# Performance work log

Hardware: AMD Instinct MI355X
Metric: run time of the kernel (lower is better)

Reference implementation:

```python
import jax, jax.numpy as jnp
import numpy as np

VOCAB, HIDDEN, BATCH, T = 32000, 256, 16, 256


def setup_inputs() -> dict:
    key = jax.random.key(0)
    ks = jax.random.split(key, 8)
    s_in = 1.0 / np.sqrt(HIDDEN)  # torch nn.RNN init scale (1/sqrt(hidden))
    inputs = jax.random.randint(ks[0], (BATCH, T), 0, VOCAB)
    targets = jax.random.randint(ks[1], (BATCH, T), 0, VOCAB)
    # RNN params: torch stores W_ih as (hidden, vocab); we keep the transpose
    # (vocab, hidden) so one_hot(x) @ W_ih.T == Wih[x] (an exact gather).
    Wih = jax.random.uniform(ks[2], (VOCAB, HIDDEN), minval=-s_in, maxval=s_in)
    bih = jax.random.uniform(ks[3], (HIDDEN,), minval=-s_in, maxval=s_in)
    Whh = jax.random.uniform(ks[4], (HIDDEN, HIDDEN), minval=-s_in, maxval=s_in)
    bhh = jax.random.uniform(ks[5], (HIDDEN,), minval=-s_in, maxval=s_in)
    Wfc = jax.random.uniform(ks[6], (VOCAB, HIDDEN), minval=-s_in, maxval=s_in)
    bfc = jax.random.uniform(ks[7], (VOCAB,), minval=-s_in, maxval=s_in)
    return {"inputs": inputs, "targets": targets, "Wih": Wih, "bih": bih,
            "Whh": Whh, "bhh": bhh, "Wfc": Wfc, "bfc": bfc}


def reference(inputs, targets, Wih, bih, Whh, bhh, Wfc, bfc):
    # one_hot(inputs) @ W_ih.T + b_ih  ==  Wih[inputs] + bih (exact same math)
    xproj = Wih[inputs] + bih                      # (B, T, H)
    B = inputs.shape[0]
    h0 = jnp.zeros((B, HIDDEN), dtype=Wih.dtype)

    def step(h, xt):
        h = jnp.tanh(xt + h @ Whh.T + bhh)
        return h, h

    _, hs = jax.lax.scan(step, h0, jnp.swapaxes(xproj, 0, 1))  # (T, B, H)
    hs = jnp.swapaxes(hs, 0, 1)                    # (B, T, H)
    logits = hs @ Wfc.T + bfc                      # (B, T, V)
    logp = jax.nn.log_softmax(logits, axis=-1)
    nll = -jnp.take_along_axis(logp, targets[..., None], axis=-1)
    return jnp.mean(nll)                           # scalar cross-entropy loss
```

## Files before the change

### kernel.cpp

```cpp
#include <hip/hip_runtime.h>
#include <hip/hip_bf16.h>
#include <stdint.h>

#define VOCAB 32000
#define HID   256
#define BATCH 16
#define SEQT  256
#define ROWS  (BATCH*SEQT)

typedef __attribute__((ext_vector_type(8))) short bf16x8_t;
typedef __attribute__((ext_vector_type(4))) float f32x4_t;

__device__ __forceinline__ short f2bs(float x) {
    __hip_bfloat16 h = __float2bfloat16(x);
    return *reinterpret_cast<short*>(&h);
}
__device__ __forceinline__ bf16x8_t cvt8(float4 a, float4 b) {
    union { short s[8]; bf16x8_t v; } u;
    u.s[0] = f2bs(a.x); u.s[1] = f2bs(a.y); u.s[2] = f2bs(a.z); u.s[3] = f2bs(a.w);
    u.s[4] = f2bs(b.x); u.s[5] = f2bs(b.y); u.s[6] = f2bs(b.z); u.s[7] = f2bs(b.w);
    return u.v;
}
__device__ __forceinline__ void barrier_lds() {
    asm volatile("s_waitcnt lgkmcnt(0)\n\ts_barrier" ::: "memory");
}
__device__ __forceinline__ float tanh_exp(float x) {
    float e = __builtin_amdgcn_exp2f(x * 2.885390081777927f);
    return fmaf(-2.f, __builtin_amdgcn_rcpf(e + 1.f), 1.f);
}
__device__ __forceinline__ uint32_t pk_bf16(float lo, float hi) {
    uint32_t r;
    asm("v_cvt_pk_bf16_f32 %0, %1, %2" : "=v"(r) : "v"(lo), "v"(hi));
    return r;
}
__device__ __forceinline__ void gload_lds16(const short* g, short* lds_base) {
    __builtin_amdgcn_global_load_lds(
        (const __attribute__((address_space(1))) void*)g,
        (__attribute__((address_space(3))) void*)lds_base, 16, 0, 0);
}


__global__ __launch_bounds__(256) void xproj_kernel(
    const int* __restrict__ inputs,
    const float* __restrict__ Wih,
    const float* __restrict__ bih,
    const float* __restrict__ bhh,
    float* __restrict__ xp,
    float* __restrict__ S)
{
    int idx = blockIdx.x * 256 + threadIdx.x;
    int h  = idx & 255;
    int tb = idx >> 8;
    int b  = tb & 15;
    int t  = tb >> 4;
    int id = inputs[b * SEQT + t];
    xp[idx] = Wih[(size_t)id * HID + h] + bih[h] + bhh[h];
    if (idx < ROWS) S[idx] = 0.0f;
}

__device__ void rnn_core(const float* __restrict__ xp,
                         const float* __restrict__ Whh,
                         __hip_bfloat16* __restrict__ hs)
{
    __shared__ __align__(8) short hbuf[2][16][264];
    const int tid = threadIdx.x;
    const int l = tid & 63, w = tid >> 6;
    const int lr = l & 15, lh = l >> 4;
    const int n0 = w * 32 + lr * 2;
    short* hsg = (short*)hs + (n0 >> 5) * 512 + (((n0 >> 3) & 3) * 128) + (n0 & 7);

    bf16x8_t bfrag[2][8];
#pragma unroll
    for (int nt = 0; nt < 2; nt++)
#pragma unroll
        for (int ki = 0; ki < 8; ki++) {
            const float4* p = (const float4*)(Whh + (size_t)(n0 + nt) * HID + ki * 32 + lh * 8);
            bfrag[nt][ki] = cvt8(p[0], p[1]);
        }
    for (int i = tid; i < 16 * 264; i += 512) ((short*)hbuf[0])[i] = 0;
    __syncthreads();

    float2 xva[4], xvb[4];
#pragma unroll
    for (int r = 0; r < 4; r++)
        xva[r] = *(const float2*)(xp + (lh * 4 + r) * HID + n0);

    auto step = [&](int SRC, int DST, float2* xc, float2* xn, int t) {
        bf16x8_t afr[8];
#pragma unroll
        for (int ki = 0; ki < 8; ki++)
            afr[ki] = *(const bf16x8_t*)(&hbuf[SRC][lr][ki * 32 + lh * 8]);

        f32x4_t a0a = {xc[0].x, xc[1].x, xc[2].x, xc[3].x};
        f32x4_t a1a = {xc[0].y, xc[1].y, xc[2].y, xc[3].y};
        f32x4_t a0b = {0.f, 0.f, 0.f, 0.f};
        f32x4_t a1b = {0.f, 0.f, 0.f, 0.f};
#pragma unroll
        for (int ki = 0; ki < 4; ki++) {
            a0a = __builtin_amdgcn_mfma_f32_16x16x32_bf16(afr[ki],     bfrag[0][ki],     a0a, 0, 0, 0);
            a0b = __builtin_amdgcn_mfma_f32_16x16x32_bf16(afr[ki + 4], bfrag[0][ki + 4], a0b, 0, 0, 0);
            a1a = __builtin_amdgcn_mfma_f32_16x16x32_bf16(afr[ki],     bfrag[1][ki],     a1a, 0, 0, 0);
            a1b = __builtin_amdgcn_mfma_f32_16x16x32_bf16(afr[ki + 4], bfrag[1][ki + 4], a1b, 0, 0, 0);
        }

        if (t + 1 < SEQT) {
            const float* xb = xp + (size_t)(t + 1) * (BATCH * HID);
#pragma unroll
            for (int r = 0; r < 4; r++)
                xn[r] = *(const float2*)(xb + (lh * 4 + r) * HID + n0);
        }

#pragma unroll
        for (int r = 0; r < 4; r++) {
            float v0 = a0a[r] + a0b[r];
            float v1 = a1a[r] + a1b[r];
            uint32_t pk = pk_bf16(tanh_exp(v0), tanh_exp(v1));
            *(uint32_t*)(&hbuf[DST][lh * 4 + r][n0]) = pk;
            *(uint32_t*)(hsg + (size_t)t * 4096 + (lh * 4 + r) * 8) = pk;
        }
        barrier_lds();
    };

    for (int t = 0; t < SEQT; t += 2) {
        step(0, 1, xva, xvb, t);
        step(1, 0, xvb, xva, t + 1);
    }
}

__global__ __launch_bounds__(512, 1) void rnncvt_kernel(
    const float* __restrict__ xp,
    const float* __restrict__ Whh,
    __hip_bfloat16* __restrict__ hs,
    const float* __restrict__ Wfc,
    __hip_bfloat16* __restrict__ Wfcb,
    int do_cvt)
{
    if (blockIdx.x == 0) { rnn_core(xp, Whh, hs); return; }
    if (!do_cvt) return;
    for (int idx = (int)(blockIdx.x - 1) * 512 + threadIdx.x;
         idx < (VOCAB * HID / 8); idx += 256 * 512) {
        int e   = idx * 8;
        int m   = (e >> 3) & 15;
        int lhh = (e >> 7) & 3;
        int ki  = (e >> 9) & 7;
        int tile = e >> 12;
        const float4* p = (const float4*)(Wfc + (size_t)(tile * 16 + m) * HID
                                          + ki * 32 + lhh * 8);
        *(bf16x8_t*)((short*)Wfcb + (size_t)e) = cvt8(p[0], p[1]);
    }
}

template <bool BF16B>
__global__ __launch_bounds__(256) void fc_kernel(
    const __hip_bfloat16* __restrict__ hsz,
    const void* __restrict__ WfcP,
    const float* __restrict__ bfc,
    const int* __restrict__ targets,
    float* __restrict__ S,
    float* __restrict__ TL)
{
    __shared__ __align__(16) short As[2][8 * 512];
    __shared__ __align__(16) short Bs[2][8 * 512];
    __shared__ int tgt[128];

    const int bid = blockIdx.x;
    const int xcd = bid & 7;
    const int j   = bid >> 3;
    const int m_id = j & 31;
    const int n_id = (j >> 5) * 8 + xcd;
    if (n_id >= VOCAB / 128) return;
    const int m0 = m_id * 128, n0 = n_id * 128;

    const int tid = threadIdx.x;
    const int l = tid & 63, w = tid >> 6;
    const int lr = l & 15, lh = l >> 4;
    const int wm = (w >> 1) * 64, wn = (w & 1) * 64;

    if (tid < 128) {
        int r = m0 + tid;
        tgt[tid] = targets[((r & 15) << 8) | (r >> 4)];
    }
    __builtin_amdgcn_sched_barrier(0);

    const short* Ag = (const short*)hsz + (size_t)m_id * 32768 + (size_t)(w * 2) * 4096 + l * 8;
    const short* Bg = (const short*)WfcP + (size_t)n_id * 32768 + (size_t)(w * 2) * 4096 + l * 8;
    const float* Bf = (const float*)WfcP;

    f32x4_t acc[4][4];
    const f32x4_t z = {0.f, 0.f, 0.f, 0.f};
#pragma unroll
    for (int i = 0; i < 4; i++)
#pragma unroll
        for (int jj = 0; jj < 4; jj++) acc[i][jj] = z;

    if (BF16B) {
        auto stage = [&](int buf, int s) {
            gload_lds16(Ag + s * 512,        &As[buf][(w * 2) * 512]);
            gload_lds16(Ag + 4096 + s * 512, &As[buf][(w * 2 + 1) * 512]);
            gload_lds16(Bg + s * 512,        &Bs[buf][(w * 2) * 512]);
            gload_lds16(Bg + 4096 + s * 512, &Bs[buf][(w * 2 + 1) * 512]);
        };
        stage(0, 0);
        stage(1, 1);
        __builtin_amdgcn_sched_barrier(0);

#pragma unroll
        for (int s = 0; s < 8; s++) {
            const int buf = s & 1;
            if (s < 7) asm volatile("s_waitcnt vmcnt(4)\n\ts_barrier" ::: "memory");
            else       asm volatile("s_waitcnt vmcnt(0)\n\ts_barrier" ::: "memory");

            bf16x8_t a[4], b[4];
#pragma unroll
            for (int mt = 0; mt < 4; mt++)
                a[mt] = *(const bf16x8_t*)&As[buf][(((w >> 1) * 4 + mt) * 512) + l * 8];
#pragma unroll
            for (int nt = 0; nt < 4; nt++)
                b[nt] = *(const bf16x8_t*)&Bs[buf][(((w & 1) * 4 + nt) * 512) + l * 8];

            if (s < 6) {
                barrier_lds();
                stage(buf, s + 2);
                __builtin_amdgcn_sched_barrier(0);
            }
#pragma unroll
            for (int mt = 0; mt < 4; mt++)
#pragma unroll
                for (int nt = 0; nt < 4; nt++)
                    acc[mt][nt] = __builtin_amdgcn_mfma_f32_16x16x32_bf16(
                        a[mt], b[nt], acc[mt][nt], 0, 0, 0);
        }
    } else {
        for (int s = 0; s < 8; s++) {
            __syncthreads();
#pragma unroll
            for (int i = 0; i < 2; i++) {
                int tt = w * 2 + i;
                bf16x8_t va = *(const bf16x8_t*)(Ag + i * 4096 + s * 512);
                *(bf16x8_t*)&As[0][tt * 512 + l * 8] = va;
                int n = n0 + tt * 16 + lr;
                const float4* p = (const float4*)(Bf + (size_t)n * HID + s * 32 + lh * 8);
                *(bf16x8_t*)&Bs[0][tt * 512 + l * 8] = cvt8(p[0], p[1]);
            }
            __syncthreads();
            bf16x8_t a[4], b[4];
#pragma unroll
            for (int mt = 0; mt < 4; mt++)
                a[mt] = *(const bf16x8_t*)&As[0][(((w >> 1) * 4 + mt) * 512) + l * 8];
#pragma unroll
            for (int nt = 0; nt < 4; nt++)
                b[nt] = *(const bf16x8_t*)&Bs[0][(((w & 1) * 4 + nt) * 512) + l * 8];
#pragma unroll
            for (int mt = 0; mt < 4; mt++)
#pragma unroll
                for (int nt = 0; nt < 4; nt++)
                    acc[mt][nt] = __builtin_amdgcn_mfma_f32_16x16x32_bf16(
                        a[mt], b[nt], acc[mt][nt], 0, 0, 0);
        }
    }

    int tg[16];
#pragma unroll
    for (int i = 0; i < 16; i++)
        tg[i] = tgt[wm + (i >> 2) * 16 + lh * 4 + (i & 3)];

    float rsum[16];
#pragma unroll
    for (int i = 0; i < 16; i++) rsum[i] = 0.f;
#pragma unroll
    for (int nt = 0; nt < 4; nt++) {
        int n = n0 + wn + nt * 16 + lr;
        float bias = bfc[n];
#pragma unroll
        for (int mt = 0; mt < 4; mt++)
#pragma unroll
            for (int r = 0; r < 4; r++) {
                float v = acc[mt][nt][r] + bias;
                rsum[mt * 4 + r] += __expf(v);
                if (tg[mt * 4 + r] == n)
                    TL[m0 + wm + mt * 16 + lh * 4 + r] = v;
            }
    }
#pragma unroll
    for (int m = 1; m < 16; m <<= 1)
#pragma unroll
        for (int i = 0; i < 16; i++) rsum[i] += __shfl_xor(rsum[i], m, 64);
    if (lr == 0) {
#pragma unroll
        for (int i = 0; i < 16; i++) {
            int r = m0 + wm + (i >> 2) * 16 + lh * 4 + (i & 3);
            atomicAdd(&S[r], rsum[i]);
        }
    }
}

__global__ __launch_bounds__(256) void loss_kernel(
    const float* __restrict__ S,
    const float* __restrict__ TL,
    float* __restrict__ out)
{
    int tid = threadIdx.x;
    float p = 0.f;
    for (int i = tid; i < ROWS; i += 256) p += __logf(S[i]) - TL[i];
#pragma unroll
    for (int m = 1; m < 64; m <<= 1) p += __shfl_xor(p, m, 64);
    __shared__ float red[4];
    if ((tid & 63) == 0) red[tid >> 6] = p;
    __syncthreads();
    if (tid == 0)
        out[0] = (red[0] + red[1] + red[2] + red[3]) / (float)ROWS;
}

extern "C" void kernel_launch(void* const* d_in, const int* in_sizes, int n_in,
                              void* d_out, int out_size, void* d_ws, size_t ws_size,
                              hipStream_t stream)
{
    (void)in_sizes; (void)n_in; (void)out_size;
    const int*   inputs  = (const int*)d_in[0];
    const int*   targets = (const int*)d_in[1];
    const float* Wih = (const float*)d_in[2];
    const float* bih = (const float*)d_in[3];
    const float* Whh = (const float*)d_in[4];
    const float* bhh = (const float*)d_in[5];
    const float* Wfc = (const float*)d_in[6];
    const float* bfc = (const float*)d_in[7];

    float* S  = (float*)d_ws;
    float* TL = S + ROWS;
    float* xp = TL + ROWS;
    __hip_bfloat16* hs = (__hip_bfloat16*)(xp + (size_t)SEQT * BATCH * HID);
    __hip_bfloat16* Wfcb = hs + (size_t)ROWS * HID;

    const size_t need = (size_t)(2 * ROWS) * 4 + (size_t)ROWS * HID * 4
                      + (size_t)ROWS * HID * 2 + (size_t)VOCAB * HID * 2;
    const int use_bf16b = (ws_size >= need) ? 1 : 0;

    xproj_kernel<<<(SEQT * BATCH * HID) / 256, 256, 0, stream>>>(
        inputs, Wih, bih, bhh, xp, S);
    rnncvt_kernel<<<257, 512, 0, stream>>>(xp, Whh, hs, Wfc, Wfcb, use_bf16b);
    if (use_bf16b)
        fc_kernel<true><<<8192, 256, 0, stream>>>(hs, (const void*)Wfcb, bfc, targets, S, TL);
    else
        fc_kernel<false><<<8192, 256, 0, stream>>>(hs, (const void*)Wfc, bfc, targets, S, TL);
    loss_kernel<<<1, 256, 0, stream>>>(S, TL, (float*)d_out);
}
```

Measured before the change: 442.1 us.

## Use weight-stationary FC kernel with per-block partial sums and two-stage loss reduction

Replaces the 8192-block tiled FC GEMM with a 250-block kernel. Each block keeps its 128-column slice of the bf16 Wfc in registers and streams all hidden-state rows through double-buffered LDS. Softmax denominators are accumulated per block in LDS, written as per-block partials into the reused xp buffer, and reduced by two new loss kernels, which removes the global atomics and the repeated B-tile reloads. The RNN also now writes hs to global with coalesced 16-byte stores one step late, read back from LDS, instead of scattered 4-byte stores. The trade-offs are only 250 blocks of parallelism, high register pressure, and an extra launch.

```diff
diff --git a/kernel.cpp b/kernel.cpp
--- a/kernel.cpp
+++ b/kernel.cpp
@@ -62,12 +62,14 @@
                          const float* __restrict__ Whh,
                          __hip_bfloat16* __restrict__ hs)
 {
-    __shared__ __align__(8) short hbuf[2][16][264];
+    __shared__ short hbuf[2][16][264];
     const int tid = threadIdx.x;
     const int l = tid & 63, w = tid >> 6;
     const int lr = l & 15, lh = l >> 4;
+    const int cm = tid >> 5;
+    const int cc = (tid & 31) * 8;
     const int n0 = w * 32 + lr * 2;
-    short* hsg = (short*)hs + (n0 >> 5) * 512 + (((n0 >> 3) & 3) * 128) + (n0 & 7);
+    const int cpoff = ((cc >> 5) * 512) + (((cc >> 3) & 3) * 128) + cm * 8;
 
     bf16x8_t bfrag[2][8];
 #pragma unroll
@@ -86,6 +88,10 @@
         xva[r] = *(const float2*)(xp + (lh * 4 + r) * HID + n0);
 
     auto step = [&](int SRC, int DST, float2* xc, float2* xn, int t) {
+        if (t > 0) {
+            bf16x8_t hv = *(const bf16x8_t*)(&hbuf[SRC][cm][cc]);
+            *(bf16x8_t*)((short*)hs + (size_t)(t - 1) * 4096 + cpoff) = hv;
+        }
         bf16x8_t afr[8];
 #pragma unroll
         for (int ki = 0; ki < 8; ki++)
@@ -116,7 +122,6 @@
             float v1 = a1a[r] + a1b[r];
             uint32_t pk = pk_bf16(tanh_exp(v0), tanh_exp(v1));
             *(uint32_t*)(&hbuf[DST][lh * 4 + r][n0]) = pk;
-            *(uint32_t*)(hsg + (size_t)t * 4096 + (lh * 4 + r) * 8) = pk;
         }
         barrier_lds();
     };
@@ -125,6 +130,8 @@
         step(0, 1, xva, xvb, t);
         step(1, 0, xvb, xva, t + 1);
     }
+    bf16x8_t hv = *(const bf16x8_t*)(&hbuf[0][cm][cc]);
+    *(bf16x8_t*)((short*)hs + (size_t)(SEQT - 1) * 4096 + cpoff) = hv;
 }
 
 __global__ __launch_bounds__(512, 1) void rnncvt_kernel(
@@ -150,17 +157,164 @@
     }
 }
 
-template <bool BF16B>
-__global__ __launch_bounds__(256) void fc_kernel(
+__global__ __launch_bounds__(512, 1) void fc_sb_kernel(
     const __hip_bfloat16* __restrict__ hsz,
-    const void* __restrict__ WfcP,
+    const __hip_bfloat16* __restrict__ Wfcb,
+    const float* __restrict__ bfc,
+    const int* __restrict__ targets,
+    float* __restrict__ Sp,
+    float* __restrict__ TL)
+{
+    __shared__ __align__(16) short As[2 * 4 * 8 * 512];
+    __shared__ float rsum[ROWS];
+    __shared__ int tgtb[2][64];
+
+    const int j = blockIdx.x;
+    const int tid = threadIdx.x;
+    const int l = tid & 63, w = tid >> 6;
+    const int lr = l & 15, lh = l >> 4;
+    const int wr = w >> 1;
+    const int wc = w & 1;
+
+    bf16x8_t Br0[8], Br1[8], Br2[8], Br3[8];
+    {
+        const short* BW = (const short*)Wfcb + (size_t)(j * 8 + wc * 4) * 4096 + l * 8;
+#pragma unroll
+        for (int ki = 0; ki < 8; ki++) {
+            Br0[ki] = *(const bf16x8_t*)(BW + 0 * 4096 + ki * 512);
+            Br1[ki] = *(const bf16x8_t*)(BW + 1 * 4096 + ki * 512);
+            Br2[ki] = *(const bf16x8_t*)(BW + 2 * 4096 + ki * 512);
+            Br3[ki] = *(const bf16x8_t*)(BW + 3 * 4096 + ki * 512);
+        }
+    }
+    const int colbase = j * 128 + wc * 64 + lr;
+    const float bias0 = bfc[colbase];
+    const float bias1 = bfc[colbase + 16];
+    const float bias2 = bfc[colbase + 32];
+    const float bias3 = bfc[colbase + 48];
+
+    for (int i = tid; i < ROWS; i += 512) rsum[i] = 0.f;
+
+    const short* AG = (const short*)hsz;
+    auto stageA = [&](int buf, int m) {
+        const short* src = AG + ((size_t)(m * 4 + wr) * 8 + wc * 4) * 512 + l * 8;
+        short* dst = As + ((buf * 4 + wr) * 8 + wc * 4) * 512;
+#pragma unroll
+        for (int q = 0; q < 4; q++)
+            gload_lds16(src + q * 512, dst + q * 512);
+    };
+
+    stageA(0, 0);
+    if (tid < 64) tgtb[0][tid] = targets[((tid & 15) << 8) | (tid >> 4)];
+    __syncthreads();
+
+    for (int m = 0; m < 64; m++) {
+        const int buf = m & 1;
+        int tnext = 0;
+        if (m < 63) {
+            stageA(buf ^ 1, m + 1);
+            if (tid < 64) {
+                int row = (m + 1) * 64 + tid;
+                tnext = targets[((row & 15) << 8) | (row >> 4)];
+            }
+        }
+
+        f32x4_t acc0 = {0,0,0,0}, acc1 = {0,0,0,0}, acc2 = {0,0,0,0}, acc3 = {0,0,0,0};
+        const short* Ab = As + ((buf * 4 + wr) * 8) * 512 + l * 8;
+#pragma unroll
+        for (int ki = 0; ki < 8; ki++) {
+            bf16x8_t a = *(const bf16x8_t*)(Ab + ki * 512);
+            acc0 = __builtin_amdgcn_mfma_f32_16x16x32_bf16(a, Br0[ki], acc0, 0, 0, 0);
+            acc1 = __builtin_amdgcn_mfma_f32_16x16x32_bf16(a, Br1[ki], acc1, 0, 0, 0);
+            acc2 = __builtin_amdgcn_mfma_f32_16x16x32_bf16(a, Br2[ki], acc2, 0, 0, 0);
+            acc3 = __builtin_amdgcn_mfma_f32_16x16x32_bf16(a, Br3[ki], acc3, 0, 0, 0);
+        }
+
+        const int rowbase = m * 64 + wr * 16 + lh * 4;
+        int4 tg = *(const int4*)&tgtb[buf][wr * 16 + lh * 4];
+        float rs0 = 0.f, rs1 = 0.f, rs2 = 0.f, rs3 = 0.f;
+
+#define FC_EPI(ACC, BIAS, OFF) {                                         \
+        int col = colbase + OFF;                                         \
+        float v0 = ACC[0] + BIAS, v1 = ACC[1] + BIAS;                    \
+        float v2 = ACC[2] + BIAS, v3 = ACC[3] + BIAS;                    \
+        rs0 += __expf(v0); rs1 += __expf(v1);                            \
+        rs2 += __expf(v2); rs3 += __expf(v3);                            \
+        if (tg.x == col) TL[rowbase + 0] = v0;                           \
+        if (tg.y == col) TL[rowbase + 1] = v1;                           \
+        if (tg.z == col) TL[rowbase + 2] = v2;                           \
+        if (tg.w == col) TL[rowbase + 3] = v3; }
+
+        FC_EPI(acc0, bias0, 0)
+        FC_EPI(acc1, bias1, 16)
+        FC_EPI(acc2, bias2, 32)
+        FC_EPI(acc3, bias3, 48)
+#undef FC_EPI
+
+#pragma unroll
+        for (int d = 1; d < 16; d <<= 1) {
+            rs0 += __shfl_xor(rs0, d, 64);
+            rs1 += __shfl_xor(rs1, d, 64);
+            rs2 += __shfl_xor(rs2, d, 64);
+            rs3 += __shfl_xor(rs3, d, 64);
+        }
+        if (lr == 0) {
+            atomicAdd(&rsum[rowbase + 0], rs0);
+            atomicAdd(&rsum[rowbase + 1], rs1);
+            atomicAdd(&rsum[rowbase + 2], rs2);
+            atomicAdd(&rsum[rowbase + 3], rs3);
+        }
+
+        if (m < 63) {
+            if (tid < 64) tgtb[buf ^ 1][tid] = tnext;
+            __syncthreads();
+        }
+    }
+    __syncthreads();
+    float* SpRow = Sp + (size_t)j * ROWS;
+    *(float4*)(SpRow + tid * 8)     = *(const float4*)(rsum + tid * 8);
+    *(float4*)(SpRow + tid * 8 + 4) = *(const float4*)(rsum + tid * 8 + 4);
+}
+
+__global__ __launch_bounds__(256) void loss1_kernel(
+    const float* __restrict__ Sp,
+    const float* __restrict__ TL,
+    float* __restrict__ part)
+{
+    const int tid = threadIdx.x;
+    const int r = blockIdx.x * 256 + tid;
+    float tot = 0.f;
+#pragma unroll 5
+    for (int jj = 0; jj < 250; jj++) tot += Sp[(size_t)jj * ROWS + r];
+    float val = __logf(tot) - TL[r];
+#pragma unroll
+    for (int d = 1; d < 64; d <<= 1) val += __shfl_xor(val, d, 64);
+    __shared__ float red[4];
+    if ((tid & 63) == 0) red[tid >> 6] = val;
+    __syncthreads();
+    if (tid == 0)
+        part[blockIdx.x] = red[0] + red[1] + red[2] + red[3];
+}
+__global__ __launch_bounds__(64) void loss2_kernel(
+    const float* __restrict__ part, float* __restrict__ out)
+{
+    int tid = threadIdx.x;
+    float p = (tid < 16) ? part[tid] : 0.f;
+#pragma unroll
+    for (int d = 1; d < 64; d <<= 1) p += __shfl_xor(p, d, 64);
+    if (tid == 0) out[0] = p / (float)ROWS;
+}
+
+__global__ __launch_bounds__(256) void fc_fb_kernel(
+    const __hip_bfloat16* __restrict__ hsz,
+    const float* __restrict__ Bf,
     const float* __restrict__ bfc,
     const int* __restrict__ targets,
     float* __restrict__ S,
     float* __restrict__ TL)
 {
-    __shared__ __align__(16) short As[2][8 * 512];
-    __shared__ __align__(16) short Bs[2][8 * 512];
+    __shared__ __align__(16) short As[8 * 512];
+    __shared__ __align__(16) short Bs[8 * 512];
     __shared__ int tgt[128];
 
     const int bid = blockIdx.x;
@@ -180,11 +334,7 @@
         int r = m0 + tid;
         tgt[tid] = targets[((r & 15) << 8) | (r >> 4)];
     }
-    __builtin_amdgcn_sched_barrier(0);
-
     const short* Ag = (const short*)hsz + (size_t)m_id * 32768 + (size_t)(w * 2) * 4096 + l * 8;
-    const short* Bg = (const short*)WfcP + (size_t)n_id * 32768 + (size_t)(w * 2) * 4096 + l * 8;
-    const float* Bf = (const float*)WfcP;
 
     f32x4_t acc[4][4];
     const f32x4_t z = {0.f, 0.f, 0.f, 0.f};
@@ -193,77 +343,37 @@
 #pragma unroll
         for (int jj = 0; jj < 4; jj++) acc[i][jj] = z;
 
-    if (BF16B) {
-        auto stage = [&](int buf, int s) {
-            gload_lds16(Ag + s * 512,        &As[buf][(w * 2) * 512]);
-            gload_lds16(Ag + 4096 + s * 512, &As[buf][(w * 2 + 1) * 512]);
-            gload_lds16(Bg + s * 512,        &Bs[buf][(w * 2) * 512]);
-            gload_lds16(Bg + 4096 + s * 512, &Bs[buf][(w * 2 + 1) * 512]);
-        };
-        stage(0, 0);
-        stage(1, 1);
-        __builtin_amdgcn_sched_barrier(0);
-
-#pragma unroll
-        for (int s = 0; s < 8; s++) {
-            const int buf = s & 1;
-            if (s < 7) asm volatile("s_waitcnt vmcnt(4)\n\ts_barrier" ::: "memory");
-            else       asm volatile("s_waitcnt vmcnt(0)\n\ts_barrier" ::: "memory");
-
-            bf16x8_t a[4], b[4];
-#pragma unroll
-            for (int mt = 0; mt < 4; mt++)
-                a[mt] = *(const bf16x8_t*)&As[buf][(((w >> 1) * 4 + mt) * 512) + l * 8];
+    for (int s = 0; s < 8; s++) {
+        __syncthreads();
+#pragma unroll
+        for (int i = 0; i < 2; i++) {
+            int tt = w * 2 + i;
+            bf16x8_t va = *(const bf16x8_t*)(Ag + i * 4096 + s * 512);
+            *(bf16x8_t*)&As[tt * 512 + l * 8] = va;
+            int n = n0 + tt * 16 + lr;
+            const float4* p = (const float4*)(Bf + (size_t)n * HID + s * 32 + lh * 8);
+            *(bf16x8_t*)&Bs[tt * 512 + l * 8] = cvt8(p[0], p[1]);
+        }
+        __syncthreads();
+        bf16x8_t a[4], b[4];
+#pragma unroll
+        for (int mt = 0; mt < 4; mt++)
+            a[mt] = *(const bf16x8_t*)&As[(((w >> 1) * 4 + mt) * 512) + l * 8];
+#pragma unroll
+        for (int nt = 0; nt < 4; nt++)
+            b[nt] = *(const bf16x8_t*)&Bs[(((w & 1) * 4 + nt) * 512) + l * 8];
+#pragma unroll
+        for (int mt = 0; mt < 4; mt++)
 #pragma unroll
             for (int nt = 0; nt < 4; nt++)
-                b[nt] = *(const bf16x8_t*)&Bs[buf][(((w & 1) * 4 + nt) * 512) + l * 8];
-
-            if (s < 6) {
-                barrier_lds();
-                stage(buf, s + 2);
-                __builtin_amdgcn_sched_barrier(0);
-            }
-#pragma unroll
-            for (int mt = 0; mt < 4; mt++)
-#pragma unroll
-                for (int nt = 0; nt < 4; nt++)
-                    acc[mt][nt] = __builtin_amdgcn_mfma_f32_16x16x32_bf16(
-                        a[mt], b[nt], acc[mt][nt], 0, 0, 0);
-        }
-    } else {
-        for (int s = 0; s < 8; s++) {
-            __syncthreads();
-#pragma unroll
-            for (int i = 0; i < 2; i++) {
-                int tt = w * 2 + i;
-                bf16x8_t va = *(const bf16x8_t*)(Ag + i * 4096 + s * 512);
-                *(bf16x8_t*)&As[0][tt * 512 + l * 8] = va;
-                int n = n0 + tt * 16 + lr;
-                const float4* p = (const float4*)(Bf + (size_t)n * HID + s * 32 + lh * 8);
-                *(bf16x8_t*)&Bs[0][tt * 512 + l * 8] = cvt8(p[0], p[1]);
-            }
-            __syncthreads();
-            bf16x8_t a[4], b[4];
-#pragma unroll
-            for (int mt = 0; mt < 4; mt++)
-                a[mt] = *(const bf16x8_t*)&As[0][(((w >> 1) * 4 + mt) * 512) + l * 8];
-#pragma unroll
-            for (int nt = 0; nt < 4; nt++)
-                b[nt] = *(const bf16x8_t*)&Bs[0][(((w & 1) * 4 + nt) * 512) + l * 8];
-#pragma unroll
-            for (int mt = 0; mt < 4; mt++)
-#pragma unroll
-                for (int nt = 0; nt < 4; nt++)
-                    acc[mt][nt] = __builtin_amdgcn_mfma_f32_16x16x32_bf16(
-                        a[mt], b[nt], acc[mt][nt], 0, 0, 0);
-        }
+                acc[mt][nt] = __builtin_amdgcn_mfma_f32_16x16x32_bf16(
+                    a[mt], b[nt], acc[mt][nt], 0, 0, 0);
     }
 
     int tg[16];
 #pragma unroll
     for (int i = 0; i < 16; i++)
         tg[i] = tgt[wm + (i >> 2) * 16 + lh * 4 + (i & 3)];
-
     float rsum[16];
 #pragma unroll
     for (int i = 0; i < 16; i++) rsum[i] = 0.f;
@@ -328,6 +438,7 @@
     float* S  = (float*)d_ws;
     float* TL = S + ROWS;
     float* xp = TL + ROWS;
+    float* Sp = xp;
     __hip_bfloat16* hs = (__hip_bfloat16*)(xp + (size_t)SEQT * BATCH * HID);
     __hip_bfloat16* Wfcb = hs + (size_t)ROWS * HID;
 
@@ -338,9 +449,12 @@
     xproj_kernel<<<(SEQT * BATCH * HID) / 256, 256, 0, stream>>>(
         inputs, Wih, bih, bhh, xp, S);
     rnncvt_kernel<<<257, 512, 0, stream>>>(xp, Whh, hs, Wfc, Wfcb, use_bf16b);
-    if (use_bf16b)
-        fc_kernel<true><<<8192, 256, 0, stream>>>(hs, (const void*)Wfcb, bfc, targets, S, TL);
-    else
-        fc_kernel<false><<<8192, 256, 0, stream>>>(hs, (const void*)Wfc, bfc, targets, S, TL);
-    loss_kernel<<<1, 256, 0, stream>>>(S, TL, (float*)d_out);
-}
+    if (use_bf16b) {
+        fc_sb_kernel<<<250, 512, 0, stream>>>(hs, Wfcb, bfc, targets, Sp, TL);
+        loss1_kernel<<<16, 256, 0, stream>>>(Sp, TL, S);
+        loss2_kernel<<<1, 64, 0, stream>>>(S, (float*)d_out);
+    } else {
+        fc_fb_kernel<<<8192, 256, 0, stream>>>(hs, Wfc, bfc, targets, S, TL);
+        loss_kernel<<<1, 256, 0, stream>>>(S, TL, (float*)d_out);
+    }
+}
```

After: 440.4 us. Within noise of the previous version (-0.4%).

## Pipeline RNN time chunks with FC tiles across fused kernel launches

Applied to the files above, without the earlier changes.

Splits the sequential RNN into four 64-step chunks, each run by block 0 of a fused launch while the other blocks compute FC/log-softmax tiles for the previous chunk's hidden states. The FC tile grows to 128x256 with 512 threads, and hidden-state stores now go through LDS as coalesced 16-byte writes instead of scattered 4-byte writes. The goal is to hide the FC GEMM behind the latency-bound recurrence, at the cost of extra launches and reloading Whh for every chunk.

```diff
diff --git a/kernel.cpp b/kernel.cpp
--- a/kernel.cpp
+++ b/kernel.cpp
@@ -39,6 +39,10 @@
         (__attribute__((address_space(3))) void*)lds_base, 16, 0, 0);
 }
 
+
+struct RnnS { short hbuf[2][16][264]; };
+struct FcS  { short As[2][8][512]; short Bs[2][16][512]; int tgt[128]; };
+union  SMem { RnnS r; FcS f; };
 
 __global__ __launch_bounds__(256) void xproj_kernel(
     const int* __restrict__ inputs,
@@ -58,16 +62,19 @@
     if (idx < ROWS) S[idx] = 0.0f;
 }
 
-__device__ void rnn_core(const float* __restrict__ xp,
-                         const float* __restrict__ Whh,
-                         __hip_bfloat16* __restrict__ hs)
-{
-    __shared__ __align__(8) short hbuf[2][16][264];
+__device__ void rnn_chunk(const float* __restrict__ xp,
+                          const float* __restrict__ Whh,
+                          __hip_bfloat16* __restrict__ hs,
+                          int t0, int t1, RnnS& rs)
+{
+    auto& hbuf = rs.hbuf;
     const int tid = threadIdx.x;
     const int l = tid & 63, w = tid >> 6;
     const int lr = l & 15, lh = l >> 4;
+    const int cm = tid >> 5;
+    const int cc = (tid & 31) * 8;
     const int n0 = w * 32 + lr * 2;
-    short* hsg = (short*)hs + (n0 >> 5) * 512 + (((n0 >> 3) & 3) * 128) + (n0 & 7);
+    const int cpoff = ((cc >> 5) * 512) + (((cc >> 3) & 3) * 128) + cm * 8;
 
     bf16x8_t bfrag[2][8];
 #pragma unroll
@@ -77,15 +84,24 @@
             const float4* p = (const float4*)(Whh + (size_t)(n0 + nt) * HID + ki * 32 + lh * 8);
             bfrag[nt][ki] = cvt8(p[0], p[1]);
         }
-    for (int i = tid; i < 16 * 264; i += 512) ((short*)hbuf[0])[i] = 0;
+    if (t0 == 0) {
+        for (int i = tid; i < 16 * 264; i += 512) ((short*)hbuf[0])[i] = 0;
+    } else {
+        *(bf16x8_t*)(&hbuf[0][cm][cc]) =
+            *(const bf16x8_t*)((const short*)hs + (size_t)(t0 - 1) * 4096 + cpoff);
+    }
     __syncthreads();
 
     float2 xva[4], xvb[4];
 #pragma unroll
     for (int r = 0; r < 4; r++)
-        xva[r] = *(const float2*)(xp + (lh * 4 + r) * HID + n0);
+        xva[r] = *(const float2*)(xp + (size_t)t0 * (BATCH * HID) + (lh * 4 + r) * HID + n0);
 
     auto step = [&](int SRC, int DST, float2* xc, float2* xn, int t) {
+        if (t > 0) {
+            bf16x8_t hv = *(const bf16x8_t*)(&hbuf[SRC][cm][cc]);
+            *(bf16x8_t*)((short*)hs + (size_t)(t - 1) * 4096 + cpoff) = hv;
+        }
         bf16x8_t afr[8];
 #pragma unroll
         for (int ki = 0; ki < 8; ki++)
@@ -116,51 +132,170 @@
             float v1 = a1a[r] + a1b[r];
             uint32_t pk = pk_bf16(tanh_exp(v0), tanh_exp(v1));
             *(uint32_t*)(&hbuf[DST][lh * 4 + r][n0]) = pk;
-            *(uint32_t*)(hsg + (size_t)t * 4096 + (lh * 4 + r) * 8) = pk;
         }
         barrier_lds();
     };
 
-    for (int t = 0; t < SEQT; t += 2) {
+    for (int t = t0; t < t1; t += 2) {
         step(0, 1, xva, xvb, t);
         step(1, 0, xvb, xva, t + 1);
     }
-}
-
-__global__ __launch_bounds__(512, 1) void rnncvt_kernel(
+    bf16x8_t hv = *(const bf16x8_t*)(&hbuf[0][cm][cc]);
+    *(bf16x8_t*)((short*)hs + (size_t)(t1 - 1) * 4096 + cpoff) = hv;
+}
+
+__device__ void fc_tile(const __hip_bfloat16* __restrict__ hsz,
+                        const __hip_bfloat16* __restrict__ Wfcb,
+                        const float* __restrict__ bfc,
+                        const int* __restrict__ targets,
+                        float* __restrict__ S,
+                        float* __restrict__ TL,
+                        int m_id, int n2, FcS& fs)
+{
+    const int tid = threadIdx.x;
+    const int l = tid & 63, w = tid >> 6;
+    const int lr = l & 15, lh = l >> 4;
+    const int wm = (w >> 2) * 64, wn = (w & 3) * 64;
+    const int m0 = m_id * 128, n0 = n2 * 256;
+
+    asm volatile("s_waitcnt vmcnt(0) lgkmcnt(0)\n\ts_barrier" ::: "memory");
+
+    if (tid < 128) {
+        int r = m0 + tid;
+        fs.tgt[tid] = targets[((r & 15) << 8) | (r >> 4)];
+    }
+    __builtin_amdgcn_sched_barrier(0);
+
+    const short* Ag = (const short*)hsz  + (size_t)(m_id * 8 + w)   * 4096 + l * 8;
+    const short* Bg = (const short*)Wfcb + (size_t)(n2 * 16 + 2*w)  * 4096 + l * 8;
+
+    f32x4_t acc[4][4];
+    const f32x4_t z = {0.f, 0.f, 0.f, 0.f};
+#pragma unroll
+    for (int i = 0; i < 4; i++)
+#pragma unroll
+        for (int jj = 0; jj < 4; jj++) acc[i][jj] = z;
+
+    auto stage = [&](int buf, int s) {
+        gload_lds16(Ag + s * 512,        &fs.As[buf][w][0]);
+        gload_lds16(Bg + s * 512,        &fs.Bs[buf][2 * w][0]);
+        gload_lds16(Bg + 4096 + s * 512, &fs.Bs[buf][2 * w + 1][0]);
+    };
+    stage(0, 0);
+    stage(1, 1);
+    __builtin_amdgcn_sched_barrier(0);
+
+#pragma unroll
+    for (int s = 0; s < 8; s++) {
+        const int buf = s & 1;
+        if (s < 7) asm volatile("s_waitcnt vmcnt(3)\n\ts_barrier" ::: "memory");
+        else       asm volatile("s_waitcnt vmcnt(0)\n\ts_barrier" ::: "memory");
+
+        bf16x8_t a[4], b[4];
+#pragma unroll
+        for (int mt = 0; mt < 4; mt++)
+            a[mt] = *(const bf16x8_t*)&fs.As[buf][(w >> 2) * 4 + mt][l * 8];
+#pragma unroll
+        for (int nt = 0; nt < 4; nt++)
+            b[nt] = *(const bf16x8_t*)&fs.Bs[buf][(w & 3) * 4 + nt][l * 8];
+
+        if (s < 6) {
+            barrier_lds();
+            stage(buf, s + 2);
+            __builtin_amdgcn_sched_barrier(0);
+        }
+#pragma unroll
+        for (int mt = 0; mt < 4; mt++)
+#pragma unroll
+            for (int nt = 0; nt < 4; nt++)
+                acc[mt][nt] = __builtin_amdgcn_mfma_f32_16x16x32_bf16(
+                    a[mt], b[nt], acc[mt][nt], 0, 0, 0);
+    }
+
+    int tg[16];
+#pragma unroll
+    for (int i = 0; i < 16; i++)
+        tg[i] = fs.tgt[wm + (i >> 2) * 16 + lh * 4 + (i & 3)];
+
+    float rsum[16];
+#pragma unroll
+    for (int i = 0; i < 16; i++) rsum[i] = 0.f;
+#pragma unroll
+    for (int nt = 0; nt < 4; nt++) {
+        int n = n0 + wn + nt * 16 + lr;
+        float bias = bfc[n];
+#pragma unroll
+        for (int mt = 0; mt < 4; mt++)
+#pragma unroll
+            for (int r = 0; r < 4; r++) {
+                float v = acc[mt][nt][r] + bias;
+                rsum[mt * 4 + r] += __expf(v);
+                if (tg[mt * 4 + r] == n)
+                    TL[m0 + wm + mt * 16 + lh * 4 + r] = v;
+            }
+    }
+#pragma unroll
+    for (int m = 1; m < 16; m <<= 1)
+#pragma unroll
+        for (int i = 0; i < 16; i++) rsum[i] += __shfl_xor(rsum[i], m, 64);
+    if (lr == 0) {
+#pragma unroll
+        for (int i = 0; i < 16; i++) {
+            int r = m0 + wm + (i >> 2) * 16 + lh * 4 + (i & 3);
+            atomicAdd(&S[r], rsum[i]);
+        }
+    }
+}
+
+__global__ __launch_bounds__(512, 1) void fused_kernel(
     const float* __restrict__ xp,
     const float* __restrict__ Whh,
     __hip_bfloat16* __restrict__ hs,
     const float* __restrict__ Wfc,
     __hip_bfloat16* __restrict__ Wfcb,
-    int do_cvt)
-{
-    if (blockIdx.x == 0) { rnn_core(xp, Whh, hs); return; }
-    if (!do_cvt) return;
-    for (int idx = (int)(blockIdx.x - 1) * 512 + threadIdx.x;
-         idx < (VOCAB * HID / 8); idx += 256 * 512) {
-        int e   = idx * 8;
-        int m   = (e >> 3) & 15;
-        int lhh = (e >> 7) & 3;
-        int ki  = (e >> 9) & 7;
-        int tile = e >> 12;
-        const float4* p = (const float4*)(Wfc + (size_t)(tile * 16 + m) * HID
-                                          + ki * 32 + lhh * 8);
-        *(bf16x8_t*)((short*)Wfcb + (size_t)e) = cvt8(p[0], p[1]);
-    }
-}
-
-template <bool BF16B>
-__global__ __launch_bounds__(256) void fc_kernel(
+    const float* __restrict__ bfc,
+    const int* __restrict__ targets,
+    float* __restrict__ S,
+    float* __restrict__ TL,
+    int rnn_t0, int rnn_t1, int fc_mbase, int do_cvt)
+{
+    __shared__ SMem sm;
+    const int has_rnn = (rnn_t0 >= 0) ? 1 : 0;
+    if (has_rnn && blockIdx.x == 0) {
+        rnn_chunk(xp, Whh, hs, rnn_t0, rnn_t1, sm.r);
+        return;
+    }
+    const int g   = (int)blockIdx.x - has_rnn;
+    const int nfc = (int)gridDim.x - has_rnn;
+    if (do_cvt) {
+        for (int idx = g * 512 + (int)threadIdx.x; idx < (VOCAB * HID / 8); idx += nfc * 512) {
+            int e   = idx * 8;
+            int m   = (e >> 3) & 15;
+            int lhh = (e >> 7) & 3;
+            int ki  = (e >> 9) & 7;
+            int tile = e >> 12;
+            const float4* p = (const float4*)(Wfc + (size_t)(tile * 16 + m) * HID
+                                              + ki * 32 + lhh * 8);
+            *(bf16x8_t*)((short*)Wfcb + (size_t)e) = cvt8(p[0], p[1]);
+        }
+        return;
+    }
+    if (fc_mbase >= 0) {
+        for (int tt = g; tt < 8 * 125; tt += nfc)
+            fc_tile(hs, Wfcb, bfc, targets, S, TL, fc_mbase + tt / 125, tt % 125, sm.f);
+    }
+}
+
+__global__ __launch_bounds__(256) void fc_fb_kernel(
     const __hip_bfloat16* __restrict__ hsz,
-    const void* __restrict__ WfcP,
+    const float* __restrict__ Bf,
     const float* __restrict__ bfc,
     const int* __restrict__ targets,
     float* __restrict__ S,
     float* __restrict__ TL)
 {
-    __shared__ __align__(16) short As[2][8 * 512];
-    __shared__ __align__(16) short Bs[2][8 * 512];
+    __shared__ __align__(16) short As[8 * 512];
+    __shared__ __align__(16) short Bs[8 * 512];
     __shared__ int tgt[128];
 
     const int bid = blockIdx.x;
@@ -180,11 +315,7 @@
         int r = m0 + tid;
         tgt[tid] = targets[((r & 15) << 8) | (r >> 4)];
     }
-    __builtin_amdgcn_sched_barrier(0);
-
     const short* Ag = (const short*)hsz + (size_t)m_id * 32768 + (size_t)(w * 2) * 4096 + l * 8;
-    const short* Bg = (const short*)WfcP + (size_t)n_id * 32768 + (size_t)(w * 2) * 4096 + l * 8;
-    const float* Bf = (const float*)WfcP;
 
     f32x4_t acc[4][4];
     const f32x4_t z = {0.f, 0.f, 0.f, 0.f};
@@ -193,77 +324,37 @@
 #pragma unroll
         for (int jj = 0; jj < 4; jj++) acc[i][jj] = z;
 
-    if (BF16B) {
-        auto stage = [&](int buf, int s) {
-            gload_lds16(Ag + s * 512,        &As[buf][(w * 2) * 512]);
-            gload_lds16(Ag + 4096 + s * 512, &As[buf][(w * 2 + 1) * 512]);
-            gload_lds16(Bg + s * 512,        &Bs[buf][(w * 2) * 512]);
-            gload_lds16(Bg + 4096 + s * 512, &Bs[buf][(w * 2 + 1) * 512]);
-        };
-        stage(0, 0);
-        stage(1, 1);
-        __builtin_amdgcn_sched_barrier(0);
-
-#pragma unroll
-        for (int s = 0; s < 8; s++) {
-            const int buf = s & 1;
-            if (s < 7) asm volatile("s_waitcnt vmcnt(4)\n\ts_barrier" ::: "memory");
-            else       asm volatile("s_waitcnt vmcnt(0)\n\ts_barrier" ::: "memory");
-
-            bf16x8_t a[4], b[4];
-#pragma unroll
-            for (int mt = 0; mt < 4; mt++)
-                a[mt] = *(const bf16x8_t*)&As[buf][(((w >> 1) * 4 + mt) * 512) + l * 8];
+    for (int s = 0; s < 8; s++) {
+        __syncthreads();
+#pragma unroll
+        for (int i = 0; i < 2; i++) {
+            int tt = w * 2 + i;
+            bf16x8_t va = *(const bf16x8_t*)(Ag + i * 4096 + s * 512);
+            *(bf16x8_t*)&As[tt * 512 + l * 8] = va;
+            int n = n0 + tt * 16 + lr;
+            const float4* p = (const float4*)(Bf + (size_t)n * HID + s * 32 + lh * 8);
+            *(bf16x8_t*)&Bs[tt * 512 + l * 8] = cvt8(p[0], p[1]);
+        }
+        __syncthreads();
+        bf16x8_t a[4], b[4];
+#pragma unroll
+        for (int mt = 0; mt < 4; mt++)
+            a[mt] = *(const bf16x8_t*)&As[(((w >> 1) * 4 + mt) * 512) + l * 8];
+#pragma unroll
+        for (int nt = 0; nt < 4; nt++)
+            b[nt] = *(const bf16x8_t*)&Bs[(((w & 1) * 4 + nt) * 512) + l * 8];
+#pragma unroll
+        for (int mt = 0; mt < 4; mt++)
 #pragma unroll
             for (int nt = 0; nt < 4; nt++)
-                b[nt] = *(const bf16x8_t*)&Bs[buf][(((w & 1) * 4 + nt) * 512) + l * 8];
-
-            if (s < 6) {
-                barrier_lds();
-                stage(buf, s + 2);
-                __builtin_amdgcn_sched_barrier(0);
-            }
-#pragma unroll
-            for (int mt = 0; mt < 4; mt++)
-#pragma unroll
-                for (int nt = 0; nt < 4; nt++)
-                    acc[mt][nt] = __builtin_amdgcn_mfma_f32_16x16x32_bf16(
-                        a[mt], b[nt], acc[mt][nt], 0, 0, 0);
-        }
-    } else {
-        for (int s = 0; s < 8; s++) {
-            __syncthreads();
-#pragma unroll
-            for (int i = 0; i < 2; i++) {
-                int tt = w * 2 + i;
-                bf16x8_t va = *(const bf16x8_t*)(Ag + i * 4096 + s * 512);
-                *(bf16x8_t*)&As[0][tt * 512 + l * 8] = va;
-                int n = n0 + tt * 16 + lr;
-                const float4* p = (const float4*)(Bf + (size_t)n * HID + s * 32 + lh * 8);
-                *(bf16x8_t*)&Bs[0][tt * 512 + l * 8] = cvt8(p[0], p[1]);
-            }
-            __syncthreads();
-            bf16x8_t a[4], b[4];
-#pragma unroll
-            for (int mt = 0; mt < 4; mt++)
-                a[mt] = *(const bf16x8_t*)&As[0][(((w >> 1) * 4 + mt) * 512) + l * 8];
-#pragma unroll
-            for (int nt = 0; nt < 4; nt++)
-                b[nt] = *(const bf16x8_t*)&Bs[0][(((w & 1) * 4 + nt) * 512) + l * 8];
-#pragma unroll
-            for (int mt = 0; mt < 4; mt++)
-#pragma unroll
-                for (int nt = 0; nt < 4; nt++)
-                    acc[mt][nt] = __builtin_amdgcn_mfma_f32_16x16x32_bf16(
-                        a[mt], b[nt], acc[mt][nt], 0, 0, 0);
-        }
+                acc[mt][nt] = __builtin_amdgcn_mfma_f32_16x16x32_bf16(
+                    a[mt], b[nt], acc[mt][nt], 0, 0, 0);
     }
 
     int tg[16];
 #pragma unroll
     for (int i = 0; i < 16; i++)
         tg[i] = tgt[wm + (i >> 2) * 16 + lh * 4 + (i & 3)];
-
     float rsum[16];
 #pragma unroll
     for (int i = 0; i < 16; i++) rsum[i] = 0.f;
@@ -337,10 +428,19 @@
 
     xproj_kernel<<<(SEQT * BATCH * HID) / 256, 256, 0, stream>>>(
         inputs, Wih, bih, bhh, xp, S);
-    rnncvt_kernel<<<257, 512, 0, stream>>>(xp, Whh, hs, Wfc, Wfcb, use_bf16b);
-    if (use_bf16b)
-        fc_kernel<true><<<8192, 256, 0, stream>>>(hs, (const void*)Wfcb, bfc, targets, S, TL);
-    else
-        fc_kernel<false><<<8192, 256, 0, stream>>>(hs, (const void*)Wfc, bfc, targets, S, TL);
+
+    if (use_bf16b) {
+        fused_kernel<<<257, 512, 0, stream>>>(xp, Whh, hs, Wfc, Wfcb, bfc, targets,
+                                              S, TL, 0, 64, -1, 1);
+        for (int c = 1; c < 4; c++)
+            fused_kernel<<<769, 512, 0, stream>>>(xp, Whh, hs, Wfc, Wfcb, bfc, targets,
+                                                  S, TL, 64 * c, 64 * c + 64, 8 * (c - 1), 0);
+        fused_kernel<<<768, 512, 0, stream>>>(xp, Whh, hs, Wfc, Wfcb, bfc, targets,
+                                              S, TL, -1, -1, 24, 0);
+    } else {
+        fused_kernel<<<1, 512, 0, stream>>>(xp, Whh, hs, Wfc, Wfcb, bfc, targets,
+                                            S, TL, 0, SEQT, -1, 0);
+        fc_fb_kernel<<<8192, 256, 0, stream>>>(hs, Wfc, bfc, targets, S, TL);
+    }
     loss_kernel<<<1, 256, 0, stream>>>(S, TL, (float*)d_out);
 }
```

Result: slower. 891.5 us (+101.6%).
